# Kernel tuning notes

Measured on AMD Instinct MI355X. Metric: run time of the kernel, lower is better.

The kernel has to match this reference:

```python
import jax, jax.numpy as jnp
import numpy as np
from jax import lax

NEG_SLOPE = 0.01  # torch LeakyReLU default
PAD = 2           # (5-1)//2


def _depthwise_conv1d(x, w, b):
    # x: [B, C, L], w: [C, 1, K] (one filter per channel), b: [C]
    C = x.shape[1]
    y = lax.conv_general_dilated(
        x, w,
        window_strides=(1,),
        padding=[(PAD, PAD)],
        dimension_numbers=("NCH", "OIH", "NCH"),
        feature_group_count=C,
    )
    return y + b[None, :, None]


def setup_inputs() -> dict:
    key = jax.random.key(0)
    k1, k2, k3, k4, k5 = jax.random.split(key, 5)
    B, C, L, K = 128, 20, 10000, 5
    # fan_in for Conv1d(1,1,5) is 5 -> torch init bound = 1/sqrt(5)
    bound = 1.0 / np.sqrt(K)
    x = jax.random.normal(k1, (B, C, L), dtype=jnp.float32)
    w1 = jax.random.uniform(k2, (C, 1, K), jnp.float32, -bound, bound)
    b1 = jax.random.uniform(k3, (C,), jnp.float32, -bound, bound)
    w2 = jax.random.uniform(k4, (C, 1, K), jnp.float32, -bound, bound)
    b2 = jax.random.uniform(k5, (C,), jnp.float32, -bound, bound)
    return {"x": x, "w1": w1, "b1": b1, "w2": w2, "b2": b2}


def reference(x, w1, b1, w2, b2):
    # Equivalent to the per-channel Python loop: each channel c runs
    # conv1d(1->1) -> LeakyReLU -> conv1d(1->1) -> sigmoid, then gates x.
    h = _depthwise_conv1d(x, w1, b1)
    h = jnp.where(h >= 0, h, NEG_SLOPE * h)
    att = jax.nn.sigmoid(_depthwise_conv1d(h, w2, b2))
    return x * att
```

## Files before the change

kernel.cpp:

```cpp
#include <hip/hip_runtime.h>
#include <math.h>

#define BLOCK 256
#define VEC   4
#define TILE  (BLOCK * VEC)
#define KW    5

__global__ __launch_bounds__(BLOCK) void wav_attn_kernel(
    const float* __restrict__ x,
    const float* __restrict__ w1,
    const float* __restrict__ b1,
    const float* __restrict__ w2,
    const float* __restrict__ b2,
    float* __restrict__ out,
    int C, int L)
{
    __shared__ float sx[TILE + 8];
    __shared__ float sh[TILE + 4];

    const int row = blockIdx.y;
    const int c   = row % C;
    const long long base = (long long)row * L;
    const int t0  = blockIdx.x * TILE;
    const int tid = threadIdx.x;

    float W1[KW], W2[KW];
    #pragma unroll
    for (int k = 0; k < KW; ++k) {
        W1[k] = w1[c * KW + k];
        W2[k] = w2[c * KW + k];
    }
    const float B1 = b1[c];
    const float B2 = b2[c];

    {
        int j = tid * VEC;
        int g = t0 + j;
        float4 v;
        if (g + 3 < L) {
            v = *reinterpret_cast<const float4*>(x + base + g);
        } else {
            float tmp[4] = {0.f, 0.f, 0.f, 0.f};
            #pragma unroll
            for (int e = 0; e < 4; ++e)
                if (g + e < L) tmp[e] = x[base + g + e];
            v = make_float4(tmp[0], tmp[1], tmp[2], tmp[3]);
        }
        *reinterpret_cast<float4*>(&sx[4 + j]) = v;
    }
    if (tid < 4) {
        int gg = t0 - 4 + tid;
        sx[tid] = (gg >= 0 && gg < L) ? x[base + gg] : 0.f;
    } else if (tid < 8) {
        int e  = tid - 4;
        int gg = t0 + TILE + e;
        sx[TILE + 4 + e] = (gg < L) ? x[base + gg] : 0.f;
    }
    __syncthreads();

    for (int j = tid; j < TILE + 4; j += BLOCK) {
        int p = t0 - 2 + j;
        float acc = B1;
        #pragma unroll
        for (int k = 0; k < KW; ++k)
            acc = fmaf(W1[k], sx[j + k], acc);
        acc = (acc >= 0.f) ? acc : 0.01f * acc;
        sh[j] = (p >= 0 && p < L) ? acc : 0.f;
    }
    __syncthreads();

    {
        int m = tid * VEC;
        int i = t0 + m;
        if (i < L) {
            float res[4];
            #pragma unroll
            for (int e = 0; e < 4; ++e) {
                float z = B2;
                #pragma unroll
                for (int k = 0; k < KW; ++k)
                    z = fmaf(W2[k], sh[m + e + k], z);
                float s = 1.f / (1.f + __expf(-z));
                res[e] = sx[4 + m + e] * s;
            }
            if (i + 3 < L) {
                *reinterpret_cast<float4*>(out + base + i) =
                    make_float4(res[0], res[1], res[2], res[3]);
            } else {
                #pragma unroll
                for (int e = 0; e < 4; ++e)
                    if (i + e < L) out[base + i + e] = res[e];
            }
        }
    }
}

extern "C" void kernel_launch(void* const* d_in, const int* in_sizes, int n_in,
                              void* d_out, int out_size, void* d_ws, size_t ws_size,
                              hipStream_t stream) {
    const float* x  = (const float*)d_in[0];
    const float* w1 = (const float*)d_in[1];
    const float* b1 = (const float*)d_in[2];
    const float* w2 = (const float*)d_in[3];
    const float* b2 = (const float*)d_in[4];
    float* out = (float*)d_out;

    const int C = in_sizes[2];
    const int B = 128;
    const int L = in_sizes[0] / (B * C);

    dim3 grid((L + TILE - 1) / TILE, B * C);
    wav_attn_kernel<<<grid, BLOCK, 0, stream>>>(x, w1, b1, w2, b2, out, C, L);
}
```

Measured before the change: 188.8 us.

## Replace shared-memory tiling with per-thread register halo and recompute

Each thread now loads a 12-element window of x with three float4 loads directly into registers and computes the 8 intermediate LeakyReLU values it needs, instead of staging tiles and intermediates in shared memory with two barriers. Neighbouring threads recompute overlapping intermediates and re-read overlapping x (tripling L1/L2 read traffic), trading redundant ALU and cache reads for removing LDS traffic and synchronisation. The sigmoid division also becomes a hardware reciprocal approximation.

```diff
diff --git a/kernel.cpp b/kernel.cpp
--- a/kernel.cpp
+++ b/kernel.cpp
@@ -15,14 +15,11 @@
     float* __restrict__ out,
     int C, int L)
 {
-    __shared__ float sx[TILE + 8];
-    __shared__ float sh[TILE + 4];
-
     const int row = blockIdx.y;
     const int c   = row % C;
     const long long base = (long long)row * L;
-    const int t0  = blockIdx.x * TILE;
-    const int tid = threadIdx.x;
+    const int i   = blockIdx.x * TILE + threadIdx.x * VEC;
+    if (i >= L) return;
 
     float W1[KW], W2[KW];
     #pragma unroll
@@ -33,65 +30,52 @@
     const float B1 = b1[c];
     const float B2 = b2[c];
 
-    {
-        int j = tid * VEC;
-        int g = t0 + j;
-        float4 v;
-        if (g + 3 < L) {
-            v = *reinterpret_cast<const float4*>(x + base + g);
-        } else {
-            float tmp[4] = {0.f, 0.f, 0.f, 0.f};
-            #pragma unroll
-            for (int e = 0; e < 4; ++e)
-                if (g + e < L) tmp[e] = x[base + g + e];
-            v = make_float4(tmp[0], tmp[1], tmp[2], tmp[3]);
+    float a[12];
+    if (i >= 4 && i + 7 < L) {
+        float4 v0 = *reinterpret_cast<const float4*>(x + base + i - 4);
+        float4 v1 = *reinterpret_cast<const float4*>(x + base + i);
+        float4 v2 = *reinterpret_cast<const float4*>(x + base + i + 4);
+        a[0] = v0.x; a[1] = v0.y; a[2]  = v0.z; a[3]  = v0.w;
+        a[4] = v1.x; a[5] = v1.y; a[6]  = v1.z; a[7]  = v1.w;
+        a[8] = v2.x; a[9] = v2.y; a[10] = v2.z; a[11] = v2.w;
+    } else {
+        #pragma unroll
+        for (int e = 0; e < 12; ++e) {
+            int g = i - 4 + e;
+            a[e] = (g >= 0 && g < L) ? x[base + g] : 0.f;
         }
-        *reinterpret_cast<float4*>(&sx[4 + j]) = v;
     }
-    if (tid < 4) {
-        int gg = t0 - 4 + tid;
-        sx[tid] = (gg >= 0 && gg < L) ? x[base + gg] : 0.f;
-    } else if (tid < 8) {
-        int e  = tid - 4;
-        int gg = t0 + TILE + e;
-        sx[TILE + 4 + e] = (gg < L) ? x[base + gg] : 0.f;
-    }
-    __syncthreads();
 
-    for (int j = tid; j < TILE + 4; j += BLOCK) {
-        int p = t0 - 2 + j;
+    float h[8];
+    #pragma unroll
+    for (int j = 0; j < 8; ++j) {
+        int p = i + j - 2;
         float acc = B1;
         #pragma unroll
         for (int k = 0; k < KW; ++k)
-            acc = fmaf(W1[k], sx[j + k], acc);
+            acc = fmaf(W1[k], a[j + k], acc);
         acc = (acc >= 0.f) ? acc : 0.01f * acc;
-        sh[j] = (p >= 0 && p < L) ? acc : 0.f;
+        h[j] = (p >= 0 && p < L) ? acc : 0.f;
     }
-    __syncthreads();
 
-    {
-        int m = tid * VEC;
-        int i = t0 + m;
-        if (i < L) {
-            float res[4];
-            #pragma unroll
-            for (int e = 0; e < 4; ++e) {
-                float z = B2;
-                #pragma unroll
-                for (int k = 0; k < KW; ++k)
-                    z = fmaf(W2[k], sh[m + e + k], z);
-                float s = 1.f / (1.f + __expf(-z));
-                res[e] = sx[4 + m + e] * s;
-            }
-            if (i + 3 < L) {
-                *reinterpret_cast<float4*>(out + base + i) =
-                    make_float4(res[0], res[1], res[2], res[3]);
-            } else {
-                #pragma unroll
-                for (int e = 0; e < 4; ++e)
-                    if (i + e < L) out[base + i + e] = res[e];
-            }
-        }
+    float res[4];
+    #pragma unroll
+    for (int e = 0; e < 4; ++e) {
+        float z = B2;
+        #pragma unroll
+        for (int k = 0; k < KW; ++k)
+            z = fmaf(W2[k], h[e + k], z);
+        float s = __builtin_amdgcn_rcpf(1.f + __expf(-z));
+        res[e] = a[4 + e] * s;
+    }
+
+    if (i + 3 < L) {
+        *reinterpret_cast<float4*>(out + base + i) =
+            make_float4(res[0], res[1], res[2], res[3]);
+    } else {
+        #pragma unroll
+        for (int e = 0; e < 4; ++e)
+            if (i + e < L) out[base + i + e] = res[e];
     }
 }
 
```

Result: faster. 180.9 us (-4.2%).
